# Kernel tuning notes

Measured on AMD Instinct MI355X. Metric: run time of the kernel, lower is better.

Reference implementation:

```python
import jax, jax.numpy as jnp
import numpy as np

B, H, Q, K = 2, 12, 2048, 2048
D, NPOS = 128, 512


def setup_inputs() -> dict:
    key = jax.random.key(0)
    k1, k2, k3 = jax.random.split(key, 3)
    return {
        "query": jax.random.normal(k1, (B, H, Q, D), dtype=jnp.float32),
        "attn_logits": jax.random.normal(k2, (B, H, Q, K), dtype=jnp.float32),
        "pos_emb": jax.random.normal(k3, (1, D, NPOS), dtype=jnp.float32),
        "npos_max": NPOS,
    }


def reference(query, attn_logits, pos_emb, npos_max):
    # CoPE, 1D (H=None) branch.
    gates = jax.nn.sigmoid(attn_logits)                       # [b,h,q,k]
    # reversed cumsum along keys: position of each key counted from the right
    pos = jnp.flip(jnp.cumsum(jnp.flip(gates, axis=-1), axis=-1), axis=-1)
    pos = jnp.minimum(pos, jnp.float32(npos_max - 1))
    pos_ceil = jnp.ceil(pos).astype(jnp.int32)                # [b,h,q,k]
    pos_floor = jnp.floor(pos).astype(jnp.int32)
    # query @ pos_emb -> interpolation table over integer positions
    logits_int = jnp.einsum("bhqd,dn->bhqn", query, pos_emb[0])  # [b,h,q,npos]
    logits_ceil = jnp.take_along_axis(logits_int, pos_ceil, axis=-1)
    logits_floor = jnp.take_along_axis(logits_int, pos_floor, axis=-1)
    w = pos - pos_floor.astype(pos.dtype)
    return logits_ceil * w + logits_floor * (1.0 - w)
```

## Files before the change

### kernel.cpp

```cpp
#include <hip/hip_runtime.h>
#include <math.h>

#define DD    128
#define NPOS  512
#define KK    2048
#define RPB   16
#define BLK   1024

typedef __attribute__((ext_vector_type(8))) short short8_t;
typedef __attribute__((ext_vector_type(4))) float f32x4;

union BfPack {
    unsigned u[4];
    short8_t v;
};

__device__ __forceinline__ float sigmoidf_fast(float x) {
    return __builtin_amdgcn_rcpf(1.0f + __expf(-x));
}

__device__ __forceinline__ unsigned pack_bf16(float lo, float hi) {
    return (__float_as_uint(hi) & 0xffff0000u) | (__float_as_uint(lo) >> 16);
}

__global__ __launch_bounds__(BLK, 8)
void cope_kernel(const float* __restrict__ query,
                 const float* __restrict__ attn,
                 const float* __restrict__ pos_emb,
                 const int*   __restrict__ npos_max_p,
                 float* __restrict__ out)
{
    const int t    = threadIdx.x;
    const int wv   = t >> 6;
    const int lane = t & 63;

    __shared__ float s_tab[RPB][NPOS + 1];

    const size_t row_base = (size_t)blockIdx.x * RPB;

    {
        const int m  = lane & 15;
        const int g  = lane >> 4;
        const int n0 = wv * 32 + m;

        f32x4 acc0 = {0.f, 0.f, 0.f, 0.f};
        f32x4 acc1 = {0.f, 0.f, 0.f, 0.f};

        #pragma unroll
        for (int kk = 0; kk < 4; ++kk) {
            const int k0 = kk * 32 + g * 8;

            const float* qp = query + (row_base + m) * DD + k0;
            f32x4 a0 = *reinterpret_cast<const f32x4*>(qp);
            f32x4 a1 = *reinterpret_cast<const f32x4*>(qp + 4);
            BfPack af;
            af.u[0] = pack_bf16(a0.x, a0.y);
            af.u[1] = pack_bf16(a0.z, a0.w);
            af.u[2] = pack_bf16(a1.x, a1.y);
            af.u[3] = pack_bf16(a1.z, a1.w);

            const float* bp = pos_emb + (size_t)k0 * NPOS + n0;
            float b0[8], b1[8];
            #pragma unroll
            for (int j = 0; j < 8; ++j) {
                b0[j] = bp[(size_t)j * NPOS];
                b1[j] = bp[(size_t)j * NPOS + 16];
            }
            BfPack bf0, bf1;
            #pragma unroll
            for (int j = 0; j < 4; ++j) {
                bf0.u[j] = pack_bf16(b0[2 * j], b0[2 * j + 1]);
                bf1.u[j] = pack_bf16(b1[2 * j], b1[2 * j + 1]);
            }

            acc0 = __builtin_amdgcn_mfma_f32_16x16x32_bf16(af.v, bf0.v, acc0, 0, 0, 0);
            acc1 = __builtin_amdgcn_mfma_f32_16x16x32_bf16(af.v, bf1.v, acc1, 0, 0, 0);
        }

        #pragma unroll
        for (int r = 0; r < 4; ++r) {
            s_tab[g * 4 + r][n0]      = acc0[r];
            s_tab[g * 4 + r][n0 + 16] = acc1[r];
        }
        if (t < RPB) s_tab[t][NPOS] = 0.0f;
    }
    __syncthreads();

    const size_t row = row_base + wv;
    const float* arow = attn + row * (size_t)KK;
    float*       orow = out  + row * (size_t)KK;
    const float* tab  = s_tab[wv];

    const float clampv = (float)(*npos_max_p - 1);

    float suff[8][4];
    float lct[8];
    float incl[8];

    #pragma unroll
    for (int c = 0; c < 8; ++c) {
        f32x4 gv = *reinterpret_cast<const f32x4*>(arow + c * 256 + lane * 4);
        float s0 = sigmoidf_fast(gv.x);
        float s1 = sigmoidf_fast(gv.y);
        float s2 = sigmoidf_fast(gv.z);
        float s3 = sigmoidf_fast(gv.w);
        suff[c][3] = s3;
        suff[c][2] = s2 + suff[c][3];
        suff[c][1] = s1 + suff[c][2];
        suff[c][0] = s0 + suff[c][1];
        lct[c] = suff[c][0];

        float v = lct[c];
        #pragma unroll
        for (int off = 1; off < 64; off <<= 1) {
            float u = __shfl_down(v, off);
            if (lane + off < 64) v += u;
        }
        incl[c] = v;
    }

    float Tc[8];
    #pragma unroll
    for (int c = 0; c < 8; ++c) Tc[c] = __shfl(incl[c], 0);
    float offc[8];
    offc[7] = 0.0f;
    #pragma unroll
    for (int c = 6; c >= 0; --c) offc[c] = offc[c + 1] + Tc[c + 1];

    #pragma unroll
    for (int c = 0; c < 8; ++c) {
        float base = offc[c] + (incl[c] - lct[c]);
        f32x4 res;
        #pragma unroll
        for (int j = 0; j < 4; ++j) {
            float pos = fminf(suff[c][j] + base, clampv);
            int   ifl = (int)pos;
            float wgt = pos - (float)ifl;
            float lf  = tab[ifl];
            float lc  = tab[ifl + 1];
            res[j] = fmaf(wgt, lc - lf, lf);
        }
        __builtin_nontemporal_store(res, reinterpret_cast<f32x4*>(orow + c * 256 + lane * 4));
    }
}

extern "C" void kernel_launch(void* const* d_in, const int* in_sizes, int n_in,
                              void* d_out, int out_size, void* d_ws, size_t ws_size,
                              hipStream_t stream) {
    const float* query   = (const float*)d_in[0];
    const float* attn    = (const float*)d_in[1];
    const float* pos_emb = (const float*)d_in[2];
    const int*   nposp   = (const int*)d_in[3];
    float*       outp    = (float*)d_out;

    const int rows   = in_sizes[1] / KK;
    const int blocks = rows / RPB;

    cope_kernel<<<blocks, BLK, 0, stream>>>(query, attn, pos_emb, nposp, outp);
}
```

Baseline: 170.9 us.

## Split table GEMM and streaming gather into two kernels via bf16 workspace table

Splits the fused kernel in two. The first kernel computes the query·pos_emb interpolation table with MFMA and writes it to a bf16 workspace buffer. The second, a streaming kernel with 512-thread blocks covering 8 rows, loads each row's table into shared memory and does the sigmoid suffix-scan and gather. This decouples the GEMM phase from the bandwidth-bound streaming phase and shrinks the streaming blocks for better occupancy. In exchange it adds a second launch, a round trip of the table through global memory (about 25 MB of bf16), and extra bf16 rounding of the table values. If the workspace is too small, the original fused kernel still runs.

```diff
diff --git a/kernel.cpp b/kernel.cpp
--- a/kernel.cpp
+++ b/kernel.cpp
@@ -6,6 +6,8 @@
 #define KK    2048
 #define RPB   16
 #define BLK   1024
+#define SRPB  8
+#define SBLK  512
 
 typedef __attribute__((ext_vector_type(8))) short short8_t;
 typedef __attribute__((ext_vector_type(4))) float f32x4;
@@ -23,10 +25,74 @@
     return (__float_as_uint(hi) & 0xffff0000u) | (__float_as_uint(lo) >> 16);
 }
 
+__device__ __forceinline__ unsigned short bf16_trunc(float x) {
+    return (unsigned short)(__float_as_uint(x) >> 16);
+}
+
+__device__ __forceinline__ float bf16_to_f32(unsigned short u) {
+    return __uint_as_float(((unsigned)u) << 16);
+}
+
 __global__ __launch_bounds__(BLK, 8)
-void cope_kernel(const float* __restrict__ query,
+void cope_table(const float* __restrict__ query,
+                const float* __restrict__ pos_emb,
+                unsigned short* __restrict__ table)
+{
+    const int t    = threadIdx.x;
+    const int wv   = t >> 6;
+    const int lane = t & 63;
+
+    const size_t row_base = (size_t)blockIdx.x * RPB;
+
+    const int m  = lane & 15;
+    const int g  = lane >> 4;
+    const int n0 = wv * 32 + m;
+
+    f32x4 acc0 = {0.f, 0.f, 0.f, 0.f};
+    f32x4 acc1 = {0.f, 0.f, 0.f, 0.f};
+
+    #pragma unroll
+    for (int kk = 0; kk < 4; ++kk) {
+        const int k0 = kk * 32 + g * 8;
+
+        const float* qp = query + (row_base + m) * DD + k0;
+        f32x4 a0 = *reinterpret_cast<const f32x4*>(qp);
+        f32x4 a1 = *reinterpret_cast<const f32x4*>(qp + 4);
+        BfPack af;
+        af.u[0] = pack_bf16(a0.x, a0.y);
+        af.u[1] = pack_bf16(a0.z, a0.w);
+        af.u[2] = pack_bf16(a1.x, a1.y);
+        af.u[3] = pack_bf16(a1.z, a1.w);
+
+        const float* bp = pos_emb + (size_t)k0 * NPOS + n0;
+        float b0[8], b1[8];
+        #pragma unroll
+        for (int j = 0; j < 8; ++j) {
+            b0[j] = bp[(size_t)j * NPOS];
+            b1[j] = bp[(size_t)j * NPOS + 16];
+        }
+        BfPack bf0, bf1;
+        #pragma unroll
+        for (int j = 0; j < 4; ++j) {
+            bf0.u[j] = pack_bf16(b0[2 * j], b0[2 * j + 1]);
+            bf1.u[j] = pack_bf16(b1[2 * j], b1[2 * j + 1]);
+        }
+
+        acc0 = __builtin_amdgcn_mfma_f32_16x16x32_bf16(af.v, bf0.v, acc0, 0, 0, 0);
+        acc1 = __builtin_amdgcn_mfma_f32_16x16x32_bf16(af.v, bf1.v, acc1, 0, 0, 0);
+    }
+
+    #pragma unroll
+    for (int r = 0; r < 4; ++r) {
+        const size_t ro = (row_base + g * 4 + r) * (size_t)NPOS;
+        table[ro + n0]      = bf16_trunc(acc0[r]);
+        table[ro + n0 + 16] = bf16_trunc(acc1[r]);
+    }
+}
+
+__global__ __launch_bounds__(SBLK, 8)
+void cope_stream(const unsigned short* __restrict__ table,
                  const float* __restrict__ attn,
-                 const float* __restrict__ pos_emb,
                  const int*   __restrict__ npos_max_p,
                  float* __restrict__ out)
 {
@@ -34,6 +100,86 @@
     const int wv   = t >> 6;
     const int lane = t & 63;
 
+    __shared__ float s_tab[SRPB][NPOS + 1];
+
+    const size_t row  = (size_t)blockIdx.x * SRPB + wv;
+    const float* arow = attn + row * (size_t)KK;
+    float*       orow = out  + row * (size_t)KK;
+    float*       tab  = s_tab[wv];
+
+    {
+        const unsigned short* trow = table + row * (size_t)NPOS;
+        #pragma unroll
+        for (int j = 0; j < 8; ++j)
+            tab[lane + j * 64] = bf16_to_f32(trow[lane + j * 64]);
+        if (lane == 0) tab[NPOS] = 0.0f;
+    }
+
+    const float clampv = (float)(*npos_max_p - 1);
+
+    float suff[8][4];
+    float lct[8];
+    float incl[8];
+
+    #pragma unroll
+    for (int c = 0; c < 8; ++c) {
+        f32x4 gv = *reinterpret_cast<const f32x4*>(arow + c * 256 + lane * 4);
+        float s0 = sigmoidf_fast(gv.x);
+        float s1 = sigmoidf_fast(gv.y);
+        float s2 = sigmoidf_fast(gv.z);
+        float s3 = sigmoidf_fast(gv.w);
+        suff[c][3] = s3;
+        suff[c][2] = s2 + suff[c][3];
+        suff[c][1] = s1 + suff[c][2];
+        suff[c][0] = s0 + suff[c][1];
+        lct[c] = suff[c][0];
+
+        float v = lct[c];
+        #pragma unroll
+        for (int off = 1; off < 64; off <<= 1) {
+            float u = __shfl_down(v, off);
+            if (lane + off < 64) v += u;
+        }
+        incl[c] = v;
+    }
+
+    float Tc[8];
+    #pragma unroll
+    for (int c = 0; c < 8; ++c) Tc[c] = __shfl(incl[c], 0);
+    float offc[8];
+    offc[7] = 0.0f;
+    #pragma unroll
+    for (int c = 6; c >= 0; --c) offc[c] = offc[c + 1] + Tc[c + 1];
+
+    #pragma unroll
+    for (int c = 0; c < 8; ++c) {
+        float base = offc[c] + (incl[c] - lct[c]);
+        f32x4 res;
+        #pragma unroll
+        for (int j = 0; j < 4; ++j) {
+            float pos = fminf(suff[c][j] + base, clampv);
+            int   ifl = (int)pos;
+            float wgt = pos - (float)ifl;
+            float lf  = tab[ifl];
+            float lc  = tab[ifl + 1];
+            res[j] = fmaf(wgt, lc - lf, lf);
+        }
+        __builtin_nontemporal_store(res,
+            reinterpret_cast<f32x4*>(orow + c * 256 + lane * 4));
+    }
+}
+
+__global__ __launch_bounds__(BLK, 8)
+void cope_fused(const float* __restrict__ query,
+                const float* __restrict__ attn,
+                const float* __restrict__ pos_emb,
+                const int*   __restrict__ npos_max_p,
+                float* __restrict__ out)
+{
+    const int t    = threadIdx.x;
+    const int wv   = t >> 6;
+    const int lane = t & 63;
+
     __shared__ float s_tab[RPB][NPOS + 1];
 
     const size_t row_base = (size_t)blockIdx.x * RPB;
@@ -49,7 +195,6 @@
         #pragma unroll
         for (int kk = 0; kk < 4; ++kk) {
             const int k0 = kk * 32 + g * 8;
-
             const float* qp = query + (row_base + m) * DD + k0;
             f32x4 a0 = *reinterpret_cast<const f32x4*>(qp);
             f32x4 a1 = *reinterpret_cast<const f32x4*>(qp + 4);
@@ -72,7 +217,6 @@
                 bf0.u[j] = pack_bf16(b0[2 * j], b0[2 * j + 1]);
                 bf1.u[j] = pack_bf16(b1[2 * j], b1[2 * j + 1]);
             }
-
             acc0 = __builtin_amdgcn_mfma_f32_16x16x32_bf16(af.v, bf0.v, acc0, 0, 0, 0);
             acc1 = __builtin_amdgcn_mfma_f32_16x16x32_bf16(af.v, bf1.v, acc1, 0, 0, 0);
         }
@@ -153,8 +297,14 @@
     const int*   nposp   = (const int*)d_in[3];
     float*       outp    = (float*)d_out;
 
-    const int rows   = in_sizes[1] / KK;
-    const int blocks = rows / RPB;
-
-    cope_kernel<<<blocks, BLK, 0, stream>>>(query, attn, pos_emb, nposp, outp);
-}
+    const int rows = in_sizes[1] / KK;
+    const size_t table_bytes = (size_t)rows * NPOS * sizeof(unsigned short);
+
+    if (ws_size >= table_bytes) {
+        unsigned short* table = (unsigned short*)d_ws;
+        cope_table<<<rows / RPB, BLK, 0, stream>>>(query, pos_emb, table);
+        cope_stream<<<rows / SRPB, SBLK, 0, stream>>>(table, attn, nposp, outp);
+    } else {
+        cope_fused<<<rows / RPB, BLK, 0, stream>>>(query, attn, pos_emb, nposp, outp);
+    }
+}
```

Result: slower. 236.4 us (+38.3%).
